# Optimization experiments

Measured on AMD Instinct MI355X. Metric: run time of the kernel, lower is better.

## Reference

```python
import jax, jax.numpy as jnp
import numpy as np

N_NODES = 100000
N_EDGES = 1600000
C_IN = 128
C_OUT = 128


def setup_inputs() -> dict:
    key = jax.random.key(0)
    k1, k2, k3, k4, k5 = jax.random.split(key, 5)
    x = jax.random.normal(k1, (N_NODES, C_IN), dtype=jnp.float32)
    W = jax.random.normal(k2, (2 * C_IN, C_OUT), dtype=jnp.float32) * (1.0 / np.sqrt(2 * C_IN))
    b = jax.random.normal(k3, (C_OUT,), dtype=jnp.float32) * 0.01
    src = jax.random.randint(k4, (N_EDGES,), 0, N_NODES, dtype=jnp.int64 if jax.config.jax_enable_x64 else jnp.int32)
    dst = jax.random.randint(k5, (N_EDGES,), 0, N_NODES, dtype=jnp.int64 if jax.config.jax_enable_x64 else jnp.int32)
    return {"x": x, "W": W, "b": b, "src": src, "dst": dst}


def reference(x, W, b, src, dst):
    # Max-Relative graph conv: per-edge relative feature, max-aggregated per dst node.
    diff = x[dst] - x[src]                                  # [E, C]  (edge messages)
    max_diff = jax.ops.segment_max(diff, dst, num_segments=x.shape[0])  # [N, C]
    # Nodes with no incoming edges: segment_max yields -inf; zero them out.
    max_diff = jnp.where(jnp.isneginf(max_diff), jnp.zeros_like(max_diff), max_diff)
    h = jnp.concatenate([x, max_diff], axis=1)              # [N, 2C]
    return jax.nn.relu(h @ W + b)                           # Linear(2C->C_out) + ReLU
```

## Files before the change

kernel.cpp:

```cpp
#include <hip/hip_runtime.h>
#include <math.h>

#define NN 100000
#define NE 1600000
#define C 128

#define TS 4096
#define NT ((NE + TS - 1) / TS)
#define BUK ((NN + 511) >> 9)
#define NSC (BUK * NT)
#define NBS ((NSC + 2047) / 2048)

typedef __attribute__((ext_vector_type(8))) short   bf16x8;
typedef __attribute__((ext_vector_type(4))) float   f32x4;
typedef unsigned short ushort_t;
typedef unsigned int   uint_t;

__device__ inline ushort_t f2bf(float f) {
    union { float f; uint_t u; } a; a.f = f;
    uint_t r = a.u + 0x7fff + ((a.u >> 16) & 1);
    return (ushort_t)(r >> 16);
}

__global__ __launch_bounds__(256) void p1_hist(const int* __restrict__ dst,
                                               int* __restrict__ tileHistT) {
    __shared__ int h[BUK];
    const int t = threadIdx.x, tile = blockIdx.x;
    for (int i = t; i < BUK; i += 256) h[i] = 0;
    __syncthreads();
    const int base = tile * TS;
    for (int i = t; i < TS; i += 256) {
        int e = base + i;
        if (e < NE) atomicAdd(&h[dst[e] >> 9], 1);
    }
    __syncthreads();
    for (int i = t; i < BUK; i += 256) tileHistT[i * NT + tile] = h[i];
}

__global__ __launch_bounds__(256) void scan_partial(const int* __restrict__ in,
                                                    int* __restrict__ out,
                                                    int* __restrict__ blocksums,
                                                    int n) {
    __shared__ int ts[256];
    const int t = threadIdx.x;
    const int base = blockIdx.x * 2048 + t * 8;
    int c[8];
    int s = 0;
    #pragma unroll
    for (int j = 0; j < 8; ++j) {
        int i = base + j;
        c[j] = (i < n) ? in[i] : 0;
        s += c[j];
    }
    ts[t] = s;
    __syncthreads();
    for (int off = 1; off < 256; off <<= 1) {
        int add = (t >= off) ? ts[t - off] : 0;
        __syncthreads();
        ts[t] += add;
        __syncthreads();
    }
    int run = (t == 0) ? 0 : ts[t - 1];
    #pragma unroll
    for (int j = 0; j < 8; ++j) {
        int i = base + j;
        if (i < n) out[i] = run;
        run += c[j];
    }
    if (t == 255) blocksums[blockIdx.x] = ts[255];
}

__global__ __launch_bounds__(64) void scan_blocksums(const int* __restrict__ blocksums,
                                                     int* __restrict__ blockbase, int nb) {
    int lane = threadIdx.x;
    int v = (lane < nb) ? blocksums[lane] : 0;
    int incl = v;
    #pragma unroll
    for (int off = 1; off < 64; off <<= 1) {
        int nbr = __shfl_up(incl, off, 64);
        if (lane >= off) incl += nbr;
    }
    if (lane < nb) blockbase[lane] = incl - v;
}

__global__ __launch_bounds__(256) void add_base(int* __restrict__ out,
                                                const int* __restrict__ blockbase, int n) {
    int i = blockIdx.x * 256 + threadIdx.x;
    if (i < n) out[i] += blockbase[i >> 11];
}

__global__ __launch_bounds__(256) void p3_scatter(const int* __restrict__ dst,
                                                  const int* __restrict__ src,
                                                  const int* __restrict__ tileScan,
                                                  int2* __restrict__ coarse) {
    __shared__ int cur[BUK];
    const int t = threadIdx.x, tile = blockIdx.x;
    for (int i = t; i < BUK; i += 256) cur[i] = tileScan[i * NT + tile];
    __syncthreads();
    const int base = tile * TS;
    for (int i = t; i < TS; i += 256) {
        int e = base + i;
        if (e < NE) {
            int d = dst[e];
            int p = atomicAdd(&cur[d >> 9], 1);
            coarse[p] = make_int2(d, src[e]);
        }
    }
}

__global__ __launch_bounds__(256) void p4_build(const int2* __restrict__ coarse,
                                                const int* __restrict__ tileScan,
                                                int* __restrict__ offs,
                                                int* __restrict__ ssrc) {
    __shared__ int cnt[512];
    __shared__ int ts[256];
    const int b = blockIdx.x, t = threadIdx.x;
    const int n0 = b << 9;
    const int bs = tileScan[b * NT];
    const int be = (b == BUK - 1) ? NE : tileScan[(b + 1) * NT];
    cnt[t] = 0; cnt[t + 256] = 0;
    __syncthreads();
    for (int i = bs + t; i < be; i += 256)
        atomicAdd(&cnt[coarse[i].x - n0], 1);
    __syncthreads();
    int c0 = cnt[2 * t], c1 = cnt[2 * t + 1];
    ts[t] = c0 + c1;
    __syncthreads();
    for (int off = 1; off < 256; off <<= 1) {
        int add = (t >= off) ? ts[t - off] : 0;
        __syncthreads();
        ts[t] += add;
        __syncthreads();
    }
    int ex = (t == 0) ? 0 : ts[t - 1];
    int o0 = bs + ex, o1 = o0 + c0;
    cnt[2 * t] = o0; cnt[2 * t + 1] = o1;
    if (n0 + 2 * t < NN)     offs[n0 + 2 * t]     = o0;
    if (n0 + 2 * t + 1 < NN) offs[n0 + 2 * t + 1] = o1;
    if (b == BUK - 1 && t == 0) offs[NN] = NE;
    __syncthreads();
    for (int i = bs + t; i < be; i += 256) {
        int2 pr = coarse[i];
        int p = atomicAdd(&cnt[pr.x - n0], 1);
        ssrc[p] = pr.y;
    }
}

__global__ __launch_bounds__(256) void prep_xh(const float* __restrict__ x,
                                               ushort_t* __restrict__ xh) {
    int i = blockIdx.x * 256 + threadIdx.x;
    if (i >= NN * C / 8) return;
    int node = i >> 4;
    int c0   = (i & 15) * 8;
    const float4* xp = (const float4*)(x + (long)i * 8);
    float4 v0 = xp[0], v1 = xp[1];
    ushort_t o[8] = { f2bf(v0.x), f2bf(v0.y), f2bf(v0.z), f2bf(v0.w),
                      f2bf(v1.x), f2bf(v1.y), f2bf(v1.z), f2bf(v1.w) };
    *(bf16x8*)(xh + (long)node * 256 + c0) = *(bf16x8*)o;
}

__global__ __launch_bounds__(256) void conv_w(const float* __restrict__ W,
                                              ushort_t* __restrict__ Wt) {
    int i = blockIdx.x * 256 + threadIdx.x;
    if (i >= 2 * C * C) return;
    int k = i >> 7, n = i & 127;
    Wt[n * 256 + k] = f2bf(W[i]);
}

__global__ __launch_bounds__(256) void node_min_bf16(
        const int* __restrict__ offs, const int* __restrict__ ssrc,
        ushort_t* __restrict__ xh) {
    int wid  = (blockIdx.x * 256 + threadIdx.x) >> 6;
    int lane = threadIdx.x & 63;
    if (wid >= NN) return;
    const int beg = offs[wid], end = offs[wid + 1];
    const uint_t* xp = (const uint_t*)xh;
    float m0 = INFINITY, m1 = INFINITY;
    int i = beg;
    for (; i + 4 <= end; i += 4) {
        uint_t a0 = xp[(long)ssrc[i]     * 128 + lane];
        uint_t a1 = xp[(long)ssrc[i + 1] * 128 + lane];
        uint_t a2 = xp[(long)ssrc[i + 2] * 128 + lane];
        uint_t a3 = xp[(long)ssrc[i + 3] * 128 + lane];
        m0 = fminf(m0, fminf(fminf(__uint_as_float(a0 << 16), __uint_as_float(a1 << 16)),
                             fminf(__uint_as_float(a2 << 16), __uint_as_float(a3 << 16))));
        m1 = fminf(m1, fminf(fminf(__uint_as_float(a0 & 0xffff0000u), __uint_as_float(a1 & 0xffff0000u)),
                             fminf(__uint_as_float(a2 & 0xffff0000u), __uint_as_float(a3 & 0xffff0000u))));
    }
    for (; i < end; ++i) {
        uint_t a = xp[(long)ssrc[i] * 128 + lane];
        m0 = fminf(m0, __uint_as_float(a << 16));
        m1 = fminf(m1, __uint_as_float(a & 0xffff0000u));
    }
    uint_t xd = xp[(long)wid * 128 + lane];
    float d0 = 0.0f, d1 = 0.0f;
    if (end > beg) {
        d0 = __uint_as_float(xd << 16)         - m0;
        d1 = __uint_as_float(xd & 0xffff0000u) - m1;
    }
    uint_t packed = (uint_t)f2bf(d0) | ((uint_t)f2bf(d1) << 16);
    ((uint_t*)xh)[(long)wid * 128 + 64 + lane] = packed;
}

__global__ __launch_bounds__(256) void gemm_mfma(
        const ushort_t* __restrict__ xh, const ushort_t* __restrict__ Wt,
        const float* __restrict__ b, float* __restrict__ out) {
    const int w  = threadIdx.x >> 6;
    const int l  = threadIdx.x & 63;
    const int m0 = blockIdx.x * 64 + w * 16;
    int arow = m0 + (l & 15);
    if (arow >= NN) arow = NN - 1;
    const int kb = (l >> 4) * 8;

    f32x4 acc[8];
    #pragma unroll
    for (int n = 0; n < 8; ++n) acc[n] = (f32x4){0.f, 0.f, 0.f, 0.f};

    const ushort_t* ap    = xh + (long)arow * 256 + kb;
    const ushort_t* wbase = Wt + (l & 15) * 256 + kb;

    #pragma unroll
    for (int k0 = 0; k0 < 256; k0 += 32) {
        bf16x8 a = *(const bf16x8*)(ap + k0);
        #pragma unroll
        for (int n = 0; n < 8; ++n) {
            bf16x8 bb = *(const bf16x8*)(wbase + n * 16 * 256 + k0);
            acc[n] = __builtin_amdgcn_mfma_f32_16x16x32_bf16(a, bb, acc[n], 0, 0, 0);
        }
    }

    const int colb  = l & 15;
    const int rbase = m0 + ((l >> 4) << 2);
    #pragma unroll
    for (int n = 0; n < 8; ++n) {
        int col = n * 16 + colb;
        float bv = b[col];
        #pragma unroll
        for (int j = 0; j < 4; ++j) {
            int r = rbase + j;
            if (r < NN) out[(long)r * 128 + col] = fmaxf(acc[n][j] + bv, 0.0f);
        }
    }
}

__global__ void init_neginf(float* __restrict__ p, int n) {
    int i = blockIdx.x * blockDim.x + threadIdx.x;
    if (i < n) p[i] = -INFINITY;
}

__device__ inline void amaxf(float* a, float v, float cur) {
    if (cur >= v) return;
    if (v >= 0.0f) atomicMax((int*)a, __float_as_int(v));
    else           atomicMin((unsigned int*)a, __float_as_uint(v));
}

__global__ __launch_bounds__(256) void edge_max(
        const float* __restrict__ x, const int* __restrict__ src,
        const int* __restrict__ dst, float* __restrict__ maxdiff) {
    long tid = (long)blockIdx.x * blockDim.x + threadIdx.x;
    int e = (int)(tid >> 5);
    if (e >= NE) return;
    int lane = (int)(tid & 31);
    int s = src[e], d = dst[e];
    int c0 = lane * 4;
    const float4 xd = *(const float4*)(x + (long)d * C + c0);
    const float4 xs = *(const float4*)(x + (long)s * C + c0);
    float4 df;
    df.x = xd.x - xs.x; df.y = xd.y - xs.y;
    df.z = xd.z - xs.z; df.w = xd.w - xs.w;
    float* o = maxdiff + (long)d * C + c0;
    float4 cur = *(const float4*)o;
    amaxf(o + 0, df.x, cur.x);
    amaxf(o + 1, df.y, cur.y);
    amaxf(o + 2, df.z, cur.z);
    amaxf(o + 3, df.w, cur.w);
}

#define TN 32
__global__ __launch_bounds__(256) void gemm_relu(
        const float* __restrict__ x, const float* __restrict__ W,
        const float* __restrict__ b, float* __restrict__ out) {
    __shared__ float h[TN][2 * C];
    const int nb = blockIdx.x * TN;
    const int t  = threadIdx.x;
    for (int i = t; i < TN * 2 * C / 4; i += 256) {
        int idx  = i * 4;
        int node = idx / (2 * C);
        int ci   = idx % (2 * C);
        float4 v;
        if (ci < C) {
            v = *(const float4*)(x + (long)(nb + node) * C + ci);
        } else {
            v = *(const float4*)(out + (long)(nb + node) * C + (ci - C));
            if (v.x == -INFINITY) v.x = 0.0f;
            if (v.y == -INFINITY) v.y = 0.0f;
            if (v.z == -INFINITY) v.z = 0.0f;
            if (v.w == -INFINITY) v.w = 0.0f;
        }
        *(float4*)&h[node][ci] = v;
    }
    __syncthreads();
    const int co = (t & 31) * 4;
    const int n0 = (t >> 5) * 4;
    float acc[4][4];
    #pragma unroll
    for (int i = 0; i < 4; ++i)
        #pragma unroll
        for (int j = 0; j < 4; ++j) acc[i][j] = 0.0f;
    for (int ci = 0; ci < 2 * C; ++ci) {
        float4 w = *(const float4*)(W + (long)ci * C + co);
        #pragma unroll
        for (int i = 0; i < 4; ++i) {
            float hv = h[n0 + i][ci];
            acc[i][0] = fmaf(hv, w.x, acc[i][0]);
            acc[i][1] = fmaf(hv, w.y, acc[i][1]);
            acc[i][2] = fmaf(hv, w.z, acc[i][2]);
            acc[i][3] = fmaf(hv, w.w, acc[i][3]);
        }
    }
    float4 bias = *(const float4*)(b + co);
    #pragma unroll
    for (int i = 0; i < 4; ++i) {
        float4 r;
        r.x = fmaxf(acc[i][0] + bias.x, 0.0f);
        r.y = fmaxf(acc[i][1] + bias.y, 0.0f);
        r.z = fmaxf(acc[i][2] + bias.z, 0.0f);
        r.w = fmaxf(acc[i][3] + bias.w, 0.0f);
        *(float4*)(out + (long)(nb + n0 + i) * C + co) = r;
    }
}

extern "C" void kernel_launch(void* const* d_in, const int* in_sizes, int n_in,
                              void* d_out, int out_size, void* d_ws, size_t ws_size,
                              hipStream_t stream) {
    const float* x   = (const float*)d_in[0];
    const float* W   = (const float*)d_in[1];
    const float* b   = (const float*)d_in[2];
    const int*   src = (const int*)d_in[3];
    const int*   dst = (const int*)d_in[4];
    float* out = (float*)d_out;

    size_t ints_head = (size_t)128 + NSC + (NN + 1) + NE;
    size_t head_b    = ((ints_head * 4) + 255) & ~(size_t)255;
    size_t xh_b      = (size_t)NN * 256 * 2;
    size_t wt_b      = (size_t)2 * C * C * 2;
    size_t need      = head_b + xh_b + wt_b;

    if (ws_size >= need) {
        int* blocksums = (int*)d_ws;
        int* blockbase = blocksums + 64;
        int* tileScan  = blockbase + 64;
        int* offs      = tileScan + NSC;
        int* ssrc      = offs + NN + 1;
        ushort_t* xh   = (ushort_t*)((char*)d_ws + head_b);
        ushort_t* Wt   = (ushort_t*)((char*)d_ws + head_b + xh_b);
        int*  tileHistT = (int*)xh;
        int2* coarse    = (int2*)xh;

        p1_hist<<<NT, 256, 0, stream>>>(dst, tileHistT);
        scan_partial<<<NBS, 256, 0, stream>>>(tileHistT, tileScan, blocksums, NSC);
        scan_blocksums<<<1, 64, 0, stream>>>(blocksums, blockbase, NBS);
        add_base<<<(NSC + 255) / 256, 256, 0, stream>>>(tileScan, blockbase, NSC);
        p3_scatter<<<NT, 256, 0, stream>>>(dst, src, tileScan, coarse);
        p4_build<<<BUK, 256, 0, stream>>>(coarse, tileScan, offs, ssrc);

        prep_xh<<<(NN * C / 8 + 255) / 256, 256, 0, stream>>>(x, xh);
        conv_w<<<(2 * C * C + 255) / 256, 256, 0, stream>>>(W, Wt);
        node_min_bf16<<<NN / 4, 256, 0, stream>>>(offs, ssrc, xh);
        gemm_mfma<<<(NN + 63) / 64, 256, 0, stream>>>(xh, Wt, b, out);
    } else {
        int n = NN * C;
        init_neginf<<<(n + 255) / 256, 256, 0, stream>>>(out, n);
        long threads = (long)NE * 32;
        edge_max<<<(int)((threads + 255) / 256), 256, 0, stream>>>(x, src, dst, out);
        gemm_relu<<<(NN + TN - 1) / TN, 256, 0, stream>>>(x, W, b, out);
    }
}
```

Before: 298.7 us.

## Fuse setup kernels, pack CSR entries, and vectorize node min-gather

Merges the bf16 conversion of x, the W transpose and the dst histogram into one launch, and removes the add_base pass by adding the block base inside scatter and build. Coarse edge records shrink from int2 to a packed 32-bit word holding the local dst index and src, cutting scatter traffic. The per-node min gather now loads 16-byte chunks with four edges in flight per wave and reduces them with shuffles, replacing the 4-byte per-lane loads. The packing assumes node ids fit in 17 bits, and the output buffer is reused as scratch for the coarse records.

After: 294.4 us. About the same (-1.4%).

```diff
diff --git a/kernel.cpp b/kernel.cpp
--- a/kernel.cpp
+++ b/kernel.cpp
@@ -10,6 +10,8 @@
 #define BUK ((NN + 511) >> 9)
 #define NSC (BUK * NT)
 #define NBS ((NSC + 2047) / 2048)
+#define PREP_BLKS (NN * C / 8 / 256)
+#define CONVW_BLKS (2 * C * C / 256)
 
 typedef __attribute__((ext_vector_type(8))) short   bf16x8;
 typedef __attribute__((ext_vector_type(4))) float   f32x4;
@@ -22,19 +24,38 @@
     return (ushort_t)(r >> 16);
 }
 
-__global__ __launch_bounds__(256) void p1_hist(const int* __restrict__ dst,
-                                               int* __restrict__ tileHistT) {
+__global__ __launch_bounds__(256) void k_setup(
+        const float* __restrict__ x, ushort_t* __restrict__ xh,
+        const float* __restrict__ W, ushort_t* __restrict__ Wt,
+        const int* __restrict__ dst, int* __restrict__ tileHistT) {
     __shared__ int h[BUK];
-    const int t = threadIdx.x, tile = blockIdx.x;
-    for (int i = t; i < BUK; i += 256) h[i] = 0;
-    __syncthreads();
-    const int base = tile * TS;
-    for (int i = t; i < TS; i += 256) {
-        int e = base + i;
-        if (e < NE) atomicAdd(&h[dst[e] >> 9], 1);
-    }
-    __syncthreads();
-    for (int i = t; i < BUK; i += 256) tileHistT[i * NT + tile] = h[i];
+    const int t  = threadIdx.x;
+    const int bb = blockIdx.x;
+    if (bb < PREP_BLKS) {
+        int i = bb * 256 + t;
+        int node = i >> 4;
+        int c0   = (i & 15) * 8;
+        const float4* xp = (const float4*)(x + (long)i * 8);
+        float4 v0 = xp[0], v1 = xp[1];
+        ushort_t o[8] = { f2bf(v0.x), f2bf(v0.y), f2bf(v0.z), f2bf(v0.w),
+                          f2bf(v1.x), f2bf(v1.y), f2bf(v1.z), f2bf(v1.w) };
+        *(bf16x8*)(xh + (long)node * 256 + c0) = *(bf16x8*)o;
+    } else if (bb < PREP_BLKS + CONVW_BLKS) {
+        int i = (bb - PREP_BLKS) * 256 + t;
+        int k = i >> 7, n = i & 127;
+        Wt[n * 256 + k] = f2bf(W[i]);
+    } else {
+        const int tile = bb - PREP_BLKS - CONVW_BLKS;
+        for (int i = t; i < BUK; i += 256) h[i] = 0;
+        __syncthreads();
+        const int base = tile * TS;
+        for (int i = t; i < TS; i += 256) {
+            int e = base + i;
+            if (e < NE) atomicAdd(&h[dst[e] >> 9], 1);
+        }
+        __syncthreads();
+        for (int i = t; i < BUK; i += 256) tileHistT[i * NT + tile] = h[i];
+    }
 }
 
 __global__ __launch_bounds__(256) void scan_partial(const int* __restrict__ in,
@@ -83,19 +104,17 @@
     if (lane < nb) blockbase[lane] = incl - v;
 }
 
-__global__ __launch_bounds__(256) void add_base(int* __restrict__ out,
-                                                const int* __restrict__ blockbase, int n) {
-    int i = blockIdx.x * 256 + threadIdx.x;
-    if (i < n) out[i] += blockbase[i >> 11];
-}
-
 __global__ __launch_bounds__(256) void p3_scatter(const int* __restrict__ dst,
                                                   const int* __restrict__ src,
                                                   const int* __restrict__ tileScan,
-                                                  int2* __restrict__ coarse) {
+                                                  const int* __restrict__ blockbase,
+                                                  uint_t* __restrict__ coarse) {
     __shared__ int cur[BUK];
     const int t = threadIdx.x, tile = blockIdx.x;
-    for (int i = t; i < BUK; i += 256) cur[i] = tileScan[i * NT + tile];
+    for (int i = t; i < BUK; i += 256) {
+        int idx = i * NT + tile;
+        cur[i] = tileScan[idx] + blockbase[idx >> 11];
+    }
     __syncthreads();
     const int base = tile * TS;
     for (int i = t; i < TS; i += 256) {
@@ -103,25 +122,29 @@
         if (e < NE) {
             int d = dst[e];
             int p = atomicAdd(&cur[d >> 9], 1);
-            coarse[p] = make_int2(d, src[e]);
-        }
-    }
-}
-
-__global__ __launch_bounds__(256) void p4_build(const int2* __restrict__ coarse,
+            coarse[p] = ((uint_t)(d & 511) << 17) | (uint_t)src[e];
+        }
+    }
+}
+
+__global__ __launch_bounds__(256) void p4_build(const uint_t* __restrict__ coarse,
                                                 const int* __restrict__ tileScan,
+                                                const int* __restrict__ blockbase,
                                                 int* __restrict__ offs,
                                                 int* __restrict__ ssrc) {
     __shared__ int cnt[512];
     __shared__ int ts[256];
     const int b = blockIdx.x, t = threadIdx.x;
     const int n0 = b << 9;
-    const int bs = tileScan[b * NT];
-    const int be = (b == BUK - 1) ? NE : tileScan[(b + 1) * NT];
+    const int i0 = b * NT;
+    const int bs = tileScan[i0] + blockbase[i0 >> 11];
+    int be;
+    if (b == BUK - 1) be = NE;
+    else { int i1 = (b + 1) * NT; be = tileScan[i1] + blockbase[i1 >> 11]; }
     cnt[t] = 0; cnt[t + 256] = 0;
     __syncthreads();
     for (int i = bs + t; i < be; i += 256)
-        atomicAdd(&cnt[coarse[i].x - n0], 1);
+        atomicAdd(&cnt[(int)(coarse[i] >> 17)], 1);
     __syncthreads();
     int c0 = cnt[2 * t], c1 = cnt[2 * t + 1];
     ts[t] = c0 + c1;
@@ -140,66 +163,68 @@
     if (b == BUK - 1 && t == 0) offs[NN] = NE;
     __syncthreads();
     for (int i = bs + t; i < be; i += 256) {
-        int2 pr = coarse[i];
-        int p = atomicAdd(&cnt[pr.x - n0], 1);
-        ssrc[p] = pr.y;
-    }
-}
-
-__global__ __launch_bounds__(256) void prep_xh(const float* __restrict__ x,
-                                               ushort_t* __restrict__ xh) {
-    int i = blockIdx.x * 256 + threadIdx.x;
-    if (i >= NN * C / 8) return;
-    int node = i >> 4;
-    int c0   = (i & 15) * 8;
-    const float4* xp = (const float4*)(x + (long)i * 8);
-    float4 v0 = xp[0], v1 = xp[1];
-    ushort_t o[8] = { f2bf(v0.x), f2bf(v0.y), f2bf(v0.z), f2bf(v0.w),
-                      f2bf(v1.x), f2bf(v1.y), f2bf(v1.z), f2bf(v1.w) };
-    *(bf16x8*)(xh + (long)node * 256 + c0) = *(bf16x8*)o;
-}
-
-__global__ __launch_bounds__(256) void conv_w(const float* __restrict__ W,
-                                              ushort_t* __restrict__ Wt) {
-    int i = blockIdx.x * 256 + threadIdx.x;
-    if (i >= 2 * C * C) return;
-    int k = i >> 7, n = i & 127;
-    Wt[n * 256 + k] = f2bf(W[i]);
-}
-
-__global__ __launch_bounds__(256) void node_min_bf16(
+        uint_t pk = coarse[i];
+        int p = atomicAdd(&cnt[(int)(pk >> 17)], 1);
+        ssrc[p] = (int)(pk & 0x1FFFF);
+    }
+}
+
+#define ACCQ(u)  { m[0] = fminf(m[0], __uint_as_float((u).x << 16));          \
+                   m[1] = fminf(m[1], __uint_as_float((u).x & 0xffff0000u));  \
+                   m[2] = fminf(m[2], __uint_as_float((u).y << 16));          \
+                   m[3] = fminf(m[3], __uint_as_float((u).y & 0xffff0000u));  \
+                   m[4] = fminf(m[4], __uint_as_float((u).z << 16));          \
+                   m[5] = fminf(m[5], __uint_as_float((u).z & 0xffff0000u));  \
+                   m[6] = fminf(m[6], __uint_as_float((u).w << 16));          \
+                   m[7] = fminf(m[7], __uint_as_float((u).w & 0xffff0000u)); }
+
+__global__ __launch_bounds__(256) void node_min_v2(
         const int* __restrict__ offs, const int* __restrict__ ssrc,
         ushort_t* __restrict__ xh) {
-    int wid  = (blockIdx.x * 256 + threadIdx.x) >> 6;
-    int lane = threadIdx.x & 63;
+    const int wid  = (blockIdx.x * 256 + threadIdx.x) >> 6;
+    const int lane = threadIdx.x & 63;
     if (wid >= NN) return;
+    const int g = lane >> 4;
+    const int s = lane & 15;
     const int beg = offs[wid], end = offs[wid + 1];
-    const uint_t* xp = (const uint_t*)xh;
-    float m0 = INFINITY, m1 = INFINITY;
+    const char* xb = (const char*)xh;
+    float m[8];
+    #pragma unroll
+    for (int j = 0; j < 8; ++j) m[j] = INFINITY;
     int i = beg;
-    for (; i + 4 <= end; i += 4) {
-        uint_t a0 = xp[(long)ssrc[i]     * 128 + lane];
-        uint_t a1 = xp[(long)ssrc[i + 1] * 128 + lane];
-        uint_t a2 = xp[(long)ssrc[i + 2] * 128 + lane];
-        uint_t a3 = xp[(long)ssrc[i + 3] * 128 + lane];
-        m0 = fminf(m0, fminf(fminf(__uint_as_float(a0 << 16), __uint_as_float(a1 << 16)),
-                             fminf(__uint_as_float(a2 << 16), __uint_as_float(a3 << 16))));
-        m1 = fminf(m1, fminf(fminf(__uint_as_float(a0 & 0xffff0000u), __uint_as_float(a1 & 0xffff0000u)),
-                             fminf(__uint_as_float(a2 & 0xffff0000u), __uint_as_float(a3 & 0xffff0000u))));
-    }
-    for (; i < end; ++i) {
-        uint_t a = xp[(long)ssrc[i] * 128 + lane];
-        m0 = fminf(m0, __uint_as_float(a << 16));
-        m1 = fminf(m1, __uint_as_float(a & 0xffff0000u));
-    }
-    uint_t xd = xp[(long)wid * 128 + lane];
-    float d0 = 0.0f, d1 = 0.0f;
-    if (end > beg) {
-        d0 = __uint_as_float(xd << 16)         - m0;
-        d1 = __uint_as_float(xd & 0xffff0000u) - m1;
-    }
-    uint_t packed = (uint_t)f2bf(d0) | ((uint_t)f2bf(d1) << 16);
-    ((uint_t*)xh)[(long)wid * 128 + 64 + lane] = packed;
+    for (; i + 8 <= end; i += 8) {
+        int e0 = ssrc[i + g];
+        int e1 = ssrc[i + 4 + g];
+        uint4 a = *(const uint4*)(xb + (long)e0 * 512 + s * 16);
+        uint4 bq = *(const uint4*)(xb + (long)e1 * 512 + s * 16);
+        ACCQ(a);
+        ACCQ(bq);
+    }
+    for (; i < end; i += 4) {
+        int e = i + g;
+        int idx = ssrc[(e < end) ? e : (end - 1)];
+        uint4 a = *(const uint4*)(xb + (long)idx * 512 + s * 16);
+        if (e < end) ACCQ(a);
+    }
+    #pragma unroll
+    for (int j = 0; j < 8; ++j) {
+        m[j] = fminf(m[j], __shfl_xor(m[j], 16, 64));
+        m[j] = fminf(m[j], __shfl_xor(m[j], 32, 64));
+    }
+    if (g == 0) {
+        uint4 xd = *(const uint4*)(xb + (long)wid * 512 + s * 16);
+        uint_t xu[4] = { xd.x, xd.y, xd.z, xd.w };
+        bool has = end > beg;
+        uint4 o;
+        uint_t* op = (uint_t*)&o;
+        #pragma unroll
+        for (int j = 0; j < 4; ++j) {
+            float lo = has ? (__uint_as_float(xu[j] << 16)         - m[2 * j])     : 0.0f;
+            float hi = has ? (__uint_as_float(xu[j] & 0xffff0000u) - m[2 * j + 1]) : 0.0f;
+            op[j] = (uint_t)f2bf(lo) | ((uint_t)f2bf(hi) << 16);
+        }
+        *(uint4*)((char*)xh + (long)wid * 512 + 256 + s * 16) = o;
+    }
 }
 
 __global__ __launch_bounds__(256) void gemm_mfma(
@@ -354,19 +379,15 @@
         int* ssrc      = offs + NN + 1;
         ushort_t* xh   = (ushort_t*)((char*)d_ws + head_b);
         ushort_t* Wt   = (ushort_t*)((char*)d_ws + head_b + xh_b);
-        int*  tileHistT = (int*)xh;
-        int2* coarse    = (int2*)xh;
-
-        p1_hist<<<NT, 256, 0, stream>>>(dst, tileHistT);
+        int*    tileHistT = ssrc;
+        uint_t* coarse    = (uint_t*)d_out;
+
+        k_setup<<<PREP_BLKS + CONVW_BLKS + NT, 256, 0, stream>>>(x, xh, W, Wt, dst, tileHistT);
         scan_partial<<<NBS, 256, 0, stream>>>(tileHistT, tileScan, blocksums, NSC);
         scan_blocksums<<<1, 64, 0, stream>>>(blocksums, blockbase, NBS);
-        add_base<<<(NSC + 255) / 256, 256, 0, stream>>>(tileScan, blockbase, NSC);
-        p3_scatter<<<NT, 256, 0, stream>>>(dst, src, tileScan, coarse);
-        p4_build<<<BUK, 256, 0, stream>>>(coarse, tileScan, offs, ssrc);
-
-        prep_xh<<<(NN * C / 8 + 255) / 256, 256, 0, stream>>>(x, xh);
-        conv_w<<<(2 * C * C + 255) / 256, 256, 0, stream>>>(W, Wt);
-        node_min_bf16<<<NN / 4, 256, 0, stream>>>(offs, ssrc, xh);
+        p3_scatter<<<NT, 256, 0, stream>>>(dst, src, tileScan, blockbase, coarse);
+        p4_build<<<BUK, 256, 0, stream>>>(coarse, tileScan, blockbase, offs, ssrc);
+        node_min_v2<<<NN / 4, 256, 0, stream>>>(offs, ssrc, xh);
         gemm_mfma<<<(NN + 63) / 64, 256, 0, stream>>>(xh, Wt, b, out);
     } else {
         int n = NN * C;
```
